# Optimization experiments

Hardware: AMD Instinct MI355X
Metric: run time of the kernel (lower is better)

Reference implementation:

```python
import jax, jax.numpy as jnp
import numpy as np

GROUP_SIZE = 128
# AWQ nibble unpack order: reverse_awq_order = [0,4,1,5,2,6,3,7]; shifts = order*4
AWQ_SHIFTS = jnp.array([0, 16, 4, 20, 8, 24, 12, 28], dtype=jnp.int32)


def awq_dequantize(qweight, scales, qzeros, group_size=GROUP_SIZE):
    # qweight: [K, N//8] int32, scales: [K//g, N] f32, qzeros: [K//g, N//8] int32
    K = qweight.shape[0]
    N = scales.shape[1]
    # unpack 8 4-bit values per int32 in AWQ order -> [K, N]
    w = ((qweight[:, :, None] >> AWQ_SHIFTS) & 15).reshape(K, N).astype(scales.dtype)
    z = ((qzeros[:, :, None] >> AWQ_SHIFTS) & 15).reshape(-1, N).astype(scales.dtype)
    # broadcast per-group scales/zeros along the K (row) axis
    z_full = jnp.repeat(z, group_size, axis=0)       # [K, N]
    s_full = jnp.repeat(scales, group_size, axis=0)  # [K, N]
    return (w - z_full) * s_full                      # [K, N]


def setup_inputs() -> dict:
    key = jax.random.key(0)
    k1, k2, k3, k4 = jax.random.split(key, 4)
    K, N, g = 4096, 11008, GROUP_SIZE
    x = jax.random.normal(k1, (4096, K), dtype=jnp.float32)
    qweight = jax.random.randint(k2, (K, N // 8), 0, 2147483647, dtype=jnp.int32)
    scales = jax.random.uniform(k3, (K // g, N), dtype=jnp.float32) * 0.01
    qzeros = jax.random.randint(k4, (K // g, N // 8), 0, 2147483647, dtype=jnp.int32)
    return {"x": x, "qweight": qweight, "scales": scales, "qzeros": qzeros}


def reference(x, qweight, scales, qzeros):
    # F.linear(x, W_deq.T) == x @ W_deq, W_deq: [K, N]
    w_deq = awq_dequantize(qweight, scales, qzeros)
    return x @ w_deq  # [tokens, N]
```

## Files before the change

kernel.cpp:

```cpp
#include <hip/hip_runtime.h>
#include <hip/hip_fp16.h>
#include <stdint.h>
#include <stddef.h>

#define MM 4096
#define NN 11008
#define KK 4096
#define NQ (NN / 8)

#define BM 256
#define BN 256
#define BK 32
#define NKT (KK / BK)
#define GRID_N (NN / BN)
#define GRID_M (MM / BM)
#define NWG (GRID_N * GRID_M)

typedef _Float16 half8 __attribute__((ext_vector_type(8)));
typedef _Float16 half2v __attribute__((ext_vector_type(2)));
typedef float f32x4 __attribute__((ext_vector_type(4)));
typedef uint32_t uint4v __attribute__((ext_vector_type(4)));

union U1H2 { uint32_t u; half2v h; };
union U4H8 { uint4v u; half8 h; };

__device__ __forceinline__ void gload_lds16(const void* g, void* l) {
  __builtin_amdgcn_global_load_lds(
      (const __attribute__((address_space(1))) uint32_t*)g,
      (__attribute__((address_space(3))) uint32_t*)l, 16, 0, 0);
}

__global__ __launch_bounds__(256) void convert_x_kernel(const float* __restrict__ x,
                                                        _Float16* __restrict__ xh) {
  const int idx = (blockIdx.x * 256 + threadIdx.x) * 8;
  const float4* p = reinterpret_cast<const float4*>(x + idx);
  float4 a = p[0], b = p[1];
  U4H8 r;
  r.h[0] = (_Float16)a.x; r.h[1] = (_Float16)a.y;
  r.h[2] = (_Float16)a.z; r.h[3] = (_Float16)a.w;
  r.h[4] = (_Float16)b.x; r.h[5] = (_Float16)b.y;
  r.h[6] = (_Float16)b.z; r.h[7] = (_Float16)b.w;
  *reinterpret_cast<uint4v*>(xh + idx) = r.u;
}

__global__ __launch_bounds__(256) void dequant_w_kernel(const uint32_t* __restrict__ qw,
                                                        const float* __restrict__ sc,
                                                        const uint32_t* __restrict__ qz,
                                                        _Float16* __restrict__ w1) {
  const int T = blockIdx.x * 256 + threadIdx.x;
  const int qc = T % NQ;
  const int kb8 = T / NQ;
  const int g = kb8 >> 4;

  const uint32_t* qp = qw + (size_t)(kb8 * 8) * NQ + qc;
  uint32_t q[8];
#pragma unroll
  for (int j = 0; j < 8; ++j) q[j] = qp[(size_t)j * NQ];

  const uint32_t zq = qz[(size_t)g * NQ + qc];
  const float* sp = sc + (size_t)g * NN + qc * 8;
  float4 s0 = *reinterpret_cast<const float4*>(sp);
  float4 s1 = *reinterpret_cast<const float4*>(sp + 4);
  const float sv[8] = {s0.x, s0.y, s0.z, s0.w, s1.x, s1.y, s1.z, s1.w};

  _Float16* op = w1 + ((size_t)kb8 * NN + (size_t)qc * 8) * 8;
#pragma unroll
  for (int c = 0; c < 8; ++c) {
    const int sh = ((c >> 1) << 2) + ((c & 1) << 4);
    uint32_t zc = ((zq >> sh) & 15u) | 0x6400u;
    zc |= zc << 16;
    U1H2 uz; uz.u = zc;
    const _Float16 hs = (_Float16)sv[c];
    half2v s2 = {hs, hs};
    uint4v outp;
#pragma unroll
    for (int i = 0; i < 4; ++i) {
      const uint32_t lo = (q[2 * i] >> sh) & 15u;
      const uint32_t hi = (q[2 * i + 1] >> sh) & 15u;
      U1H2 uw; uw.u = lo | (hi << 16) | 0x64006400u;
      U1H2 ur; ur.h = (uw.h - uz.h) * s2;
      outp[i] = ur.u;
    }
    *reinterpret_cast<uint4v*>(op + c * 8) = outp;
  }
}

__global__ __launch_bounds__(512, 2)
void gemm_pipe(const _Float16* __restrict__ xh, const _Float16* __restrict__ w1,
               float* __restrict__ out) {
  __shared__ __align__(16) _Float16 As[4][BM][BK];
  __shared__ __align__(16) _Float16 Bs[4][4][BN][8];

  const int tid = threadIdx.x;
  const int lane = tid & 63;
  const int wid = tid >> 6;
  const int wm = wid >> 2;
  const int wn = wid & 3;
  const int lr = lane & 15;
  const int lq = lane >> 4;

  const int wg = blockIdx.x;
  const int xcd = wg & 7;
  const int j = wg >> 3;
  const int m0 = (xcd * 2 + (j & 1)) * BM;
  const int n0 = (j >> 1) * BN;

  const int ca0 = tid, ca1 = 512 + tid;
  const _Float16* aSrc0 = xh + (size_t)(m0 + (ca0 >> 2)) * KK + (ca0 & 3) * 8;
  const _Float16* aSrc1 = xh + (size_t)(m0 + (ca1 >> 2)) * KK + (ca1 & 3) * 8;
  const _Float16* bSrc0 = w1 + ((size_t)(ca0 >> 8) * NN + n0 + (ca0 & 255)) * 8;
  const _Float16* bSrc1 = w1 + ((size_t)(ca1 >> 8) * NN + n0 + (ca1 & 255)) * 8;
  const int ldsOffA0 = (wid * 64) * 8;
  const int ldsOffA1 = (512 + wid * 64) * 8;

  f32x4 acc[8][4];
  const f32x4 fz = {0.f, 0.f, 0.f, 0.f};
#pragma unroll
  for (int i = 0; i < 8; ++i)
#pragma unroll
    for (int jn = 0; jn < 4; ++jn) acc[i][jn] = fz;

#pragma unroll
  for (int t = 0; t < 3; ++t) {
    gload_lds16(aSrc0 + t * BK, (char*)&As[t][0][0] + ldsOffA0 * 2);
    gload_lds16(aSrc1 + t * BK, (char*)&As[t][0][0] + ldsOffA1 * 2);
    gload_lds16(bSrc0 + (size_t)t * NN * 32, (char*)&Bs[t][0][0][0] + ldsOffA0 * 2);
    gload_lds16(bSrc1 + (size_t)t * NN * 32, (char*)&Bs[t][0][0][0] + ldsOffA1 * 2);
  }
  asm volatile("s_waitcnt vmcnt(8)" ::: "memory");
  __builtin_amdgcn_s_barrier();
  __builtin_amdgcn_sched_barrier(0);

  for (int t = 0; t < NKT; ++t) {
    const int b = t & 3;
    const int s = (t + 3) & (NKT - 1);
    const int sb = s & 3;

    half8 af[4], bf[4];
#pragma unroll
    for (int mi = 0; mi < 4; ++mi)
      af[mi] = *reinterpret_cast<const half8*>(&As[b][wm * 128 + mi * 16 + lr][lq * 8]);
#pragma unroll
    for (int ni = 0; ni < 4; ++ni)
      bf[ni] = *reinterpret_cast<const half8*>(&Bs[b][lq][wn * 64 + ni * 16 + lr][0]);
    gload_lds16(aSrc0 + s * BK, (char*)&As[sb][0][0] + ldsOffA0 * 2);
    gload_lds16(aSrc1 + s * BK, (char*)&As[sb][0][0] + ldsOffA1 * 2);
    __builtin_amdgcn_s_barrier();
    asm volatile("s_waitcnt lgkmcnt(0)" ::: "memory");
    __builtin_amdgcn_sched_barrier(0);
    __builtin_amdgcn_s_setprio(1);
#pragma unroll
    for (int mi = 0; mi < 4; ++mi)
#pragma unroll
      for (int ni = 0; ni < 4; ++ni)
        acc[mi][ni] = __builtin_amdgcn_mfma_f32_16x16x32_f16(af[mi], bf[ni], acc[mi][ni], 0, 0, 0);
    __builtin_amdgcn_s_setprio(0);
    __builtin_amdgcn_s_barrier();
    __builtin_amdgcn_sched_barrier(0);

    half8 ag[4];
#pragma unroll
    for (int mi = 0; mi < 4; ++mi)
      ag[mi] = *reinterpret_cast<const half8*>(&As[b][wm * 128 + 64 + mi * 16 + lr][lq * 8]);
    gload_lds16(bSrc0 + (size_t)s * NN * 32, (char*)&Bs[sb][0][0][0] + ldsOffA0 * 2);
    gload_lds16(bSrc1 + (size_t)s * NN * 32, (char*)&Bs[sb][0][0][0] + ldsOffA1 * 2);
    __builtin_amdgcn_s_barrier();
    asm volatile("s_waitcnt lgkmcnt(0)" ::: "memory");
    __builtin_amdgcn_sched_barrier(0);
    __builtin_amdgcn_s_setprio(1);
#pragma unroll
    for (int mi = 0; mi < 4; ++mi)
#pragma unroll
      for (int ni = 0; ni < 4; ++ni)
        acc[4 + mi][ni] = __builtin_amdgcn_mfma_f32_16x16x32_f16(ag[mi], bf[ni], acc[4 + mi][ni], 0, 0, 0);
    __builtin_amdgcn_s_setprio(0);
    asm volatile("s_waitcnt vmcnt(8)" ::: "memory");
    __builtin_amdgcn_s_barrier();
    __builtin_amdgcn_sched_barrier(0);
  }

  float* op = out + (size_t)(m0 + wm * 128) * NN + (n0 + wn * 64);
#pragma unroll
  for (int mi = 0; mi < 8; ++mi)
#pragma unroll
    for (int ni = 0; ni < 4; ++ni)
#pragma unroll
      for (int i = 0; i < 4; ++i) {
        const int row = mi * 16 + lq * 4 + i;
        const int col = ni * 16 + lr;
        op[(size_t)row * NN + col] = acc[mi][ni][i];
      }
}

template <bool APRE>
__global__ __launch_bounds__(256)
void awq_gemm(const float* __restrict__ x, const _Float16* __restrict__ xh,
              const uint32_t* __restrict__ qw, const float* __restrict__ sc,
              const uint32_t* __restrict__ qz, float* __restrict__ out) {
  __shared__ __align__(16) _Float16 Asf[128 * 64];
  __shared__ __align__(16) _Float16 Bsf[128 * 64];

  const int tid = threadIdx.x;
  const int lane = tid & 63;
  const int wid = tid >> 6;
  const int wr = wid >> 1;
  const int wc = wid & 1;
  const int n0 = blockIdx.x * 128;
  const int m0 = blockIdx.y * 128;
  const int lr = lane & 15;
  const int lq = lane >> 4;

  const int bn = tid & 127;
  const int bh = tid >> 7;
  const int gn = n0 + bn;
  const int qc = gn >> 3;
  const int jj = gn & 7;
  const int shift = ((jj >> 1) << 2) + ((jj & 1) << 4);

  const int ar = tid >> 1;
  const int ah = tid & 1;

  f32x4 acc[4][4];
  const f32x4 fz = {0.f, 0.f, 0.f, 0.f};
#pragma unroll
  for (int i = 0; i < 4; ++i)
#pragma unroll
    for (int jn = 0; jn < 4; ++jn) acc[i][jn] = fz;

  half2v zsp = {(_Float16)0.f, (_Float16)0.f};
  half2v ssp = {(_Float16)0.f, (_Float16)0.f};

  for (int kt = 0; kt < KK / 64; ++kt) {
    const int k0 = kt * 64;
    if ((kt & 1) == 0) {
      const int g = k0 >> 7;
      const uint32_t zq = qz[(size_t)g * NQ + qc];
      uint32_t zm = ((zq >> shift) & 15u) | 0x6400u;
      zm |= zm << 16;
      U1H2 uz; uz.u = zm; zsp = uz.h;
      const float s = sc[(size_t)g * NN + gn];
      const _Float16 hs = (_Float16)s;
      ssp[0] = hs; ssp[1] = hs;
    }
    __syncthreads();
    if (APRE) {
#pragma unroll
      for (int i = 0; i < 4; ++i) {
        const int cbase = (i * 4 + wid) * 64;
        const int chunk = cbase + lane;
        const int mrow = chunk >> 3;
        const int slot = (chunk & 7) ^ (mrow & 7);
        const _Float16* gp = xh + (size_t)(m0 + mrow) * KK + k0 + slot * 8;
        gload_lds16(gp, (void*)&Asf[cbase * 8]);
      }
    } else {
      const float* xp = x + (size_t)(m0 + ar) * KK + k0 + ah * 32;
#pragma unroll
      for (int j2 = 0; j2 < 4; ++j2) {
        float4 a4 = *reinterpret_cast<const float4*>(xp + j2 * 8);
        float4 b4 = *reinterpret_cast<const float4*>(xp + j2 * 8 + 4);
        U4H8 r;
        r.h[0] = (_Float16)a4.x; r.h[1] = (_Float16)a4.y;
        r.h[2] = (_Float16)a4.z; r.h[3] = (_Float16)a4.w;
        r.h[4] = (_Float16)b4.x; r.h[5] = (_Float16)b4.y;
        r.h[6] = (_Float16)b4.z; r.h[7] = (_Float16)b4.w;
        const int slot = (ah * 4 + j2) ^ (ar & 7);
        *reinterpret_cast<uint4v*>(&Asf[ar * 64 + slot * 8]) = r.u;
      }
    }
    {
      const uint32_t* qp = qw + (size_t)(k0 + bh * 32) * NQ + qc;
#pragma unroll
      for (int f = 0; f < 4; ++f) {
        uint32_t qv[8];
#pragma unroll
        for (int jv = 0; jv < 8; ++jv) qv[jv] = qp[(size_t)(f * 8 + jv) * NQ];
        uint4v wp;
#pragma unroll
        for (int p = 0; p < 4; ++p) {
          const uint32_t lo = (qv[2 * p] >> shift) & 15u;
          const uint32_t hi = (qv[2 * p + 1] >> shift);
          const uint32_t w01 = (((hi << 16) | lo) & 0x000F000Fu) | 0x64006400u;
          U1H2 uw; uw.u = w01;
          U1H2 ur; ur.h = (uw.h - zsp) * ssp;
          wp[p] = ur.u;
        }
        const int slot = (bh * 4 + f) ^ (bn & 7);
        *reinterpret_cast<uint4v*>(&Bsf[bn * 64 + slot * 8]) = wp;
      }
    }
    __syncthreads();
#pragma unroll
    for (int kq = 0; kq < 2; ++kq) {
      half8 af[4], bf[4];
#pragma unroll
      for (int mi = 0; mi < 4; ++mi) {
        const int am = wr * 64 + mi * 16 + lr;
        const int aslot = (kq * 4 + lq) ^ (am & 7);
        af[mi] = *reinterpret_cast<const half8*>(&Asf[am * 64 + aslot * 8]);
      }
#pragma unroll
      for (int ni = 0; ni < 4; ++ni) {
        const int bn2 = wc * 64 + ni * 16 + lr;
        const int bslot = (kq * 4 + lq) ^ (bn2 & 7);
        bf[ni] = *reinterpret_cast<const half8*>(&Bsf[bn2 * 64 + bslot * 8]);
      }
#pragma unroll
      for (int mi = 0; mi < 4; ++mi)
#pragma unroll
        for (int ni = 0; ni < 4; ++ni)
          acc[mi][ni] = __builtin_amdgcn_mfma_f32_16x16x32_f16(af[mi], bf[ni], acc[mi][ni], 0, 0, 0);
    }
  }

  float* op = out + (size_t)(m0 + wr * 64) * NN + (n0 + wc * 64);
#pragma unroll
  for (int mi = 0; mi < 4; ++mi)
#pragma unroll
    for (int ni = 0; ni < 4; ++ni)
#pragma unroll
      for (int i = 0; i < 4; ++i) {
        const int row = mi * 16 + lq * 4 + i;
        const int col = ni * 16 + lr;
        op[(size_t)row * NN + col] = acc[mi][ni][i];
      }
}

extern "C" void kernel_launch(void* const* d_in, const int* in_sizes, int n_in,
                              void* d_out, int out_size, void* d_ws, size_t ws_size,
                              hipStream_t stream) {
  const float* x = (const float*)d_in[0];
  const uint32_t* qw = (const uint32_t*)d_in[1];
  const float* sc = (const float*)d_in[2];
  const uint32_t* qz = (const uint32_t*)d_in[3];
  float* out = (float*)d_out;

  const size_t xh_bytes = (size_t)MM * KK * sizeof(_Float16);
  const size_t w1_bytes = (size_t)KK * NN * sizeof(_Float16);

  if (ws_size >= xh_bytes + w1_bytes) {
    _Float16* xh = (_Float16*)d_ws;
    _Float16* w1 = (_Float16*)((char*)d_ws + xh_bytes);
    convert_x_kernel<<<(MM * KK) / (256 * 8), 256, 0, stream>>>(x, xh);
    dequant_w_kernel<<<(KK / 8) * NQ / 256, 256, 0, stream>>>(qw, sc, qz, w1);
    gemm_pipe<<<NWG, 512, 0, stream>>>(xh, w1, out);
  } else if (ws_size >= xh_bytes) {
    _Float16* xh = (_Float16*)d_ws;
    convert_x_kernel<<<(MM * KK) / (256 * 8), 256, 0, stream>>>(x, xh);
    awq_gemm<true><<<dim3(NN / 128, MM / 128), 256, 0, stream>>>(x, xh, qw, sc, qz, out);
  } else {
    awq_gemm<false><<<dim3(NN / 128, MM / 128), 256, 0, stream>>>(x, nullptr, qw, sc, qz, out);
  }
}
```

Baseline: 428.4 us.

## Pre-tile and swizzle X and dequantized W into contiguous per-tile blocks for GEMM

The conversion and dequant kernels now write fp16 X and W into a tiled, XOR-swizzled layout where each 256x32 k-tile is one contiguous 16 KB block. The pipelined GEMM then streams each tile with fully contiguous global-to-LDS loads and reads fragments from a swizzled [128][64] LDS layout to avoid bank conflicts. This targets strided global access and LDS bank conflicts in the main GEMM, at the cost of scattered writes in the prep kernels and more complex index math.

```diff
diff --git a/kernel.cpp b/kernel.cpp
--- a/kernel.cpp
+++ b/kernel.cpp
@@ -16,6 +16,8 @@
 #define GRID_M (MM / BM)
 #define NWG (GRID_N * GRID_M)
 
+#define TILE_HALFS 8192
+
 typedef _Float16 half8 __attribute__((ext_vector_type(8)));
 typedef _Float16 half2v __attribute__((ext_vector_type(2)));
 typedef float f32x4 __attribute__((ext_vector_type(4)));
@@ -28,6 +30,323 @@
   __builtin_amdgcn_global_load_lds(
       (const __attribute__((address_space(1))) uint32_t*)g,
       (__attribute__((address_space(3))) uint32_t*)l, 16, 0, 0);
+}
+
+__global__ __launch_bounds__(256) void convert_x2(const float* __restrict__ x,
+                                                  _Float16* __restrict__ xh2) {
+  const int g = blockIdx.x * 256 + threadIdx.x;
+  const int c = g & 1023;
+  const int t = (g >> 10) & 127;
+  const int pan = g >> 17;
+  const int r = c >> 3;
+  const int ps = c & 7;
+  const int u = ps ^ (r & 7);
+  const int m = pan * 256 + (u >> 2) * 128 + r;
+  const int k = t * 32 + (u & 3) * 8;
+  const float4* s = reinterpret_cast<const float4*>(x + (size_t)m * KK + k);
+  float4 a = s[0], b = s[1];
+  U4H8 o;
+  o.h[0] = (_Float16)a.x; o.h[1] = (_Float16)a.y;
+  o.h[2] = (_Float16)a.z; o.h[3] = (_Float16)a.w;
+  o.h[4] = (_Float16)b.x; o.h[5] = (_Float16)b.y;
+  o.h[6] = (_Float16)b.z; o.h[7] = (_Float16)b.w;
+  *reinterpret_cast<uint4v*>(xh2 + (size_t)g * 8) = o.u;
+}
+
+__global__ __launch_bounds__(256) void dequant_w2(const uint32_t* __restrict__ qw,
+                                                  const float* __restrict__ sc,
+                                                  const uint32_t* __restrict__ qz,
+                                                  _Float16* __restrict__ w2) {
+  const int T = blockIdx.x * 256 + threadIdx.x;
+  const int qc = T % NQ;
+  const int kb8 = T / NQ;
+  const int grp = kb8 >> 4;
+  const int t = kb8 >> 2;
+  const int kbl = kb8 & 3;
+
+  const uint32_t* qp = qw + (size_t)(kb8 * 8) * NQ + qc;
+  uint32_t q[8];
+#pragma unroll
+  for (int j = 0; j < 8; ++j) q[j] = qp[(size_t)j * NQ];
+
+  const uint32_t zq = qz[(size_t)grp * NQ + qc];
+  const float* sp = sc + (size_t)grp * NN + qc * 8;
+  float4 s0 = *reinterpret_cast<const float4*>(sp);
+  float4 s1 = *reinterpret_cast<const float4*>(sp + 4);
+  const float sv[8] = {s0.x, s0.y, s0.z, s0.w, s1.x, s1.y, s1.z, s1.w};
+
+#pragma unroll
+  for (int cc = 0; cc < 8; ++cc) {
+    const int sh = ((cc >> 1) << 2) + ((cc & 1) << 4);
+    uint32_t zc = ((zq >> sh) & 15u) | 0x6400u;
+    zc |= zc << 16;
+    U1H2 uz; uz.u = zc;
+    const _Float16 hs = (_Float16)sv[cc];
+    half2v s2 = {hs, hs};
+    uint4v outp;
+#pragma unroll
+    for (int i = 0; i < 4; ++i) {
+      const uint32_t lo = (q[2 * i] >> sh) & 15u;
+      const uint32_t hi = (q[2 * i + 1] >> sh) & 15u;
+      U1H2 uw; uw.u = lo | (hi << 16) | 0x64006400u;
+      U1H2 ur; ur.h = (uw.h - uz.h) * s2;
+      outp[i] = ur.u;
+    }
+    const int n = qc * 8 + cc;
+    const int np = n >> 8;
+    const int nn = n & 255;
+    const int r = nn & 127;
+    const int h = nn >> 7;
+    const int p = (h * 4 + kbl) ^ (r & 7);
+    const size_t chunk = (((size_t)np * 128 + t) << 10) + (r << 3) + p;
+    *reinterpret_cast<uint4v*>(w2 + chunk * 8) = outp;
+  }
+}
+
+__global__ __launch_bounds__(512, 2)
+void gemm_pipe(const _Float16* __restrict__ xh2, const _Float16* __restrict__ w2,
+               float* __restrict__ out) {
+  __shared__ __align__(16) _Float16 As[4][128][64];
+  __shared__ __align__(16) _Float16 Bs[4][128][64];
+
+  const int tid = threadIdx.x;
+  const int lane = tid & 63;
+  const int wid = tid >> 6;
+  const int wm = wid >> 2;
+  const int wn = wid & 3;
+  const int lr = lane & 15;
+  const int lq = lane >> 4;
+
+  const int wg = blockIdx.x;
+  const int xcd = wg & 7;
+  const int j = wg >> 3;
+  const int mp = xcd * 2 + (j & 1);
+  const int np = j >> 1;
+  const int m0 = mp * BM;
+  const int n0 = np * BN;
+
+  const _Float16* aT = xh2 + (size_t)mp * NKT * TILE_HALFS;
+  const _Float16* bT = w2 + (size_t)np * NKT * TILE_HALFS;
+  const size_t sOff0 = (size_t)tid * 8;
+  const size_t sOff1 = (size_t)(512 + tid) * 8;
+  const int dOff0 = wid * 1024;
+  const int dOff1 = 8192 + wid * 1024;
+
+  const int pa = (wm * 4 + lq) ^ (lr & 7);
+  const int pb = ((wn >> 1) * 4 + lq) ^ (lr & 7);
+  const int rb = (wn & 1) * 64;
+
+  f32x4 acc[8][4];
+  const f32x4 fz = {0.f, 0.f, 0.f, 0.f};
+#pragma unroll
+  for (int i = 0; i < 8; ++i)
+#pragma unroll
+    for (int jn = 0; jn < 4; ++jn) acc[i][jn] = fz;
+
+#pragma unroll
+  for (int t = 0; t < 3; ++t) {
+    gload_lds16(aT + (size_t)t * TILE_HALFS + sOff0, (char*)&As[t][0][0] + dOff0);
+    gload_lds16(aT + (size_t)t * TILE_HALFS + sOff1, (char*)&As[t][0][0] + dOff1);
+    gload_lds16(bT + (size_t)t * TILE_HALFS + sOff0, (char*)&Bs[t][0][0] + dOff0);
+    gload_lds16(bT + (size_t)t * TILE_HALFS + sOff1, (char*)&Bs[t][0][0] + dOff1);
+  }
+  asm volatile("s_waitcnt vmcnt(8)" ::: "memory");
+  __builtin_amdgcn_s_barrier();
+  __builtin_amdgcn_sched_barrier(0);
+
+  for (int t = 0; t < NKT; ++t) {
+    const int b = t & 3;
+    const int s = (t + 3) & (NKT - 1);
+    const int sb = s & 3;
+
+    half8 af[4], bf[4];
+#pragma unroll
+    for (int mi = 0; mi < 4; ++mi)
+      af[mi] = *reinterpret_cast<const half8*>(&As[b][mi * 16 + lr][pa * 8]);
+#pragma unroll
+    for (int ni = 0; ni < 4; ++ni)
+      bf[ni] = *reinterpret_cast<const half8*>(&Bs[b][rb + ni * 16 + lr][pb * 8]);
+    gload_lds16(aT + (size_t)s * TILE_HALFS + sOff0, (char*)&As[sb][0][0] + dOff0);
+    gload_lds16(aT + (size_t)s * TILE_HALFS + sOff1, (char*)&As[sb][0][0] + dOff1);
+    __builtin_amdgcn_s_barrier();
+    asm volatile("s_waitcnt lgkmcnt(0)" ::: "memory");
+    __builtin_amdgcn_sched_barrier(0);
+    __builtin_amdgcn_s_setprio(1);
+#pragma unroll
+    for (int mi = 0; mi < 4; ++mi)
+#pragma unroll
+      for (int ni = 0; ni < 4; ++ni)
+        acc[mi][ni] = __builtin_amdgcn_mfma_f32_16x16x32_f16(af[mi], bf[ni], acc[mi][ni], 0, 0, 0);
+    __builtin_amdgcn_s_setprio(0);
+    __builtin_amdgcn_s_barrier();
+    __builtin_amdgcn_sched_barrier(0);
+
+    half8 ag[4];
+#pragma unroll
+    for (int mi = 0; mi < 4; ++mi)
+      ag[mi] = *reinterpret_cast<const half8*>(&As[b][64 + mi * 16 + lr][pa * 8]);
+    gload_lds16(bT + (size_t)s * TILE_HALFS + sOff0, (char*)&Bs[sb][0][0] + dOff0);
+    gload_lds16(bT + (size_t)s * TILE_HALFS + sOff1, (char*)&Bs[sb][0][0] + dOff1);
+    __builtin_amdgcn_s_barrier();
+    asm volatile("s_waitcnt lgkmcnt(0)" ::: "memory");
+    __builtin_amdgcn_sched_barrier(0);
+    __builtin_amdgcn_s_setprio(1);
+#pragma unroll
+    for (int mi = 0; mi < 4; ++mi)
+#pragma unroll
+      for (int ni = 0; ni < 4; ++ni)
+        acc[4 + mi][ni] = __builtin_amdgcn_mfma_f32_16x16x32_f16(ag[mi], bf[ni], acc[4 + mi][ni], 0, 0, 0);
+    __builtin_amdgcn_s_setprio(0);
+    asm volatile("s_waitcnt vmcnt(8)" ::: "memory");
+    __builtin_amdgcn_s_barrier();
+    __builtin_amdgcn_sched_barrier(0);
+  }
+
+  float* op = out + (size_t)(m0 + wm * 128) * NN + (n0 + wn * 64);
+#pragma unroll
+  for (int mi = 0; mi < 8; ++mi)
+#pragma unroll
+    for (int ni = 0; ni < 4; ++ni)
+#pragma unroll
+      for (int i = 0; i < 4; ++i) {
+        const int row = mi * 16 + lq * 4 + i;
+        const int col = ni * 16 + lr;
+        op[(size_t)row * NN + col] = acc[mi][ni][i];
+      }
+}
+
+template <bool APRE>
+__global__ __launch_bounds__(256)
+void awq_gemm(const float* __restrict__ x, const _Float16* __restrict__ xh,
+              const uint32_t* __restrict__ qw, const float* __restrict__ sc,
+              const uint32_t* __restrict__ qz, float* __restrict__ out) {
+  __shared__ __align__(16) _Float16 Asf[128 * 64];
+  __shared__ __align__(16) _Float16 Bsf[128 * 64];
+
+  const int tid = threadIdx.x;
+  const int lane = tid & 63;
+  const int wid = tid >> 6;
+  const int wr = wid >> 1;
+  const int wc = wid & 1;
+  const int n0 = blockIdx.x * 128;
+  const int m0 = blockIdx.y * 128;
+  const int lr = lane & 15;
+  const int lq = lane >> 4;
+
+  const int bn = tid & 127;
+  const int bh = tid >> 7;
+  const int gn = n0 + bn;
+  const int qc = gn >> 3;
+  const int jj = gn & 7;
+  const int shift = ((jj >> 1) << 2) + ((jj & 1) << 4);
+
+  const int ar = tid >> 1;
+  const int ah = tid & 1;
+
+  f32x4 acc[4][4];
+  const f32x4 fz = {0.f, 0.f, 0.f, 0.f};
+#pragma unroll
+  for (int i = 0; i < 4; ++i)
+#pragma unroll
+    for (int jn = 0; jn < 4; ++jn) acc[i][jn] = fz;
+
+  half2v zsp = {(_Float16)0.f, (_Float16)0.f};
+  half2v ssp = {(_Float16)0.f, (_Float16)0.f};
+
+  for (int kt = 0; kt < KK / 64; ++kt) {
+    const int k0 = kt * 64;
+    if ((kt & 1) == 0) {
+      const int g = k0 >> 7;
+      const uint32_t zq = qz[(size_t)g * NQ + qc];
+      uint32_t zm = ((zq >> shift) & 15u) | 0x6400u;
+      zm |= zm << 16;
+      U1H2 uz; uz.u = zm; zsp = uz.h;
+      const float s = sc[(size_t)g * NN + gn];
+      const _Float16 hs = (_Float16)s;
+      ssp[0] = hs; ssp[1] = hs;
+    }
+    __syncthreads();
+    if (APRE) {
+#pragma unroll
+      for (int i = 0; i < 4; ++i) {
+        const int cbase = (i * 4 + wid) * 64;
+        const int chunk = cbase + lane;
+        const int mrow = chunk >> 3;
+        const int slot = (chunk & 7) ^ (mrow & 7);
+        const _Float16* gp = xh + (size_t)(m0 + mrow) * KK + k0 + slot * 8;
+        gload_lds16(gp, (void*)&Asf[cbase * 8]);
+      }
+    } else {
+      const float* xp = x + (size_t)(m0 + ar) * KK + k0 + ah * 32;
+#pragma unroll
+      for (int j2 = 0; j2 < 4; ++j2) {
+        float4 a4 = *reinterpret_cast<const float4*>(xp + j2 * 8);
+        float4 b4 = *reinterpret_cast<const float4*>(xp + j2 * 8 + 4);
+        U4H8 r;
+        r.h[0] = (_Float16)a4.x; r.h[1] = (_Float16)a4.y;
+        r.h[2] = (_Float16)a4.z; r.h[3] = (_Float16)a4.w;
+        r.h[4] = (_Float16)b4.x; r.h[5] = (_Float16)b4.y;
+        r.h[6] = (_Float16)b4.z; r.h[7] = (_Float16)b4.w;
+        const int slot = (ah * 4 + j2) ^ (ar & 7);
+        *reinterpret_cast<uint4v*>(&Asf[ar * 64 + slot * 8]) = r.u;
+      }
+    }
+    {
+      const uint32_t* qp = qw + (size_t)(k0 + bh * 32) * NQ + qc;
+#pragma unroll
+      for (int f = 0; f < 4; ++f) {
+        uint32_t qv[8];
+#pragma unroll
+        for (int jv = 0; jv < 8; ++jv) qv[jv] = qp[(size_t)(f * 8 + jv) * NQ];
+        uint4v wp;
+#pragma unroll
+        for (int p = 0; p < 4; ++p) {
+          const uint32_t lo = (qv[2 * p] >> shift) & 15u;
+          const uint32_t hi = (qv[2 * p + 1] >> shift);
+          const uint32_t w01 = (((hi << 16) | lo) & 0x000F000Fu) | 0x64006400u;
+          U1H2 uw; uw.u = w01;
+          U1H2 ur; ur.h = (uw.h - zsp) * ssp;
+          wp[p] = ur.u;
+        }
+        const int slot = (bh * 4 + f) ^ (bn & 7);
+        *reinterpret_cast<uint4v*>(&Bsf[bn * 64 + slot * 8]) = wp;
+      }
+    }
+    __syncthreads();
+#pragma unroll
+    for (int kq = 0; kq < 2; ++kq) {
+      half8 af[4], bf[4];
+#pragma unroll
+      for (int mi = 0; mi < 4; ++mi) {
+        const int am = wr * 64 + mi * 16 + lr;
+        const int aslot = (kq * 4 + lq) ^ (am & 7);
+        af[mi] = *reinterpret_cast<const half8*>(&Asf[am * 64 + aslot * 8]);
+      }
+#pragma unroll
+      for (int ni = 0; ni < 4; ++ni) {
+        const int bn2 = wc * 64 + ni * 16 + lr;
+        const int bslot = (kq * 4 + lq) ^ (bn2 & 7);
+        bf[ni] = *reinterpret_cast<const half8*>(&Bsf[bn2 * 64 + bslot * 8]);
+      }
+#pragma unroll
+      for (int mi = 0; mi < 4; ++mi)
+#pragma unroll
+        for (int ni = 0; ni < 4; ++ni)
+          acc[mi][ni] = __builtin_amdgcn_mfma_f32_16x16x32_f16(af[mi], bf[ni], acc[mi][ni], 0, 0, 0);
+    }
+  }
+
+  float* op = out + (size_t)(m0 + wr * 64) * NN + (n0 + wc * 64);
+#pragma unroll
+  for (int mi = 0; mi < 4; ++mi)
+#pragma unroll
+    for (int ni = 0; ni < 4; ++ni)
+#pragma unroll
+      for (int i = 0; i < 4; ++i) {
+        const int row = mi * 16 + lq * 4 + i;
+        const int col = ni * 16 + lr;
+        op[(size_t)row * NN + col] = acc[mi][ni][i];
+      }
 }
 
 __global__ __launch_bounds__(256) void convert_x_kernel(const float* __restrict__ x,
@@ -43,289 +362,6 @@
   *reinterpret_cast<uint4v*>(xh + idx) = r.u;
 }
 
-__global__ __launch_bounds__(256) void dequant_w_kernel(const uint32_t* __restrict__ qw,
-                                                        const float* __restrict__ sc,
-                                                        const uint32_t* __restrict__ qz,
-                                                        _Float16* __restrict__ w1) {
-  const int T = blockIdx.x * 256 + threadIdx.x;
-  const int qc = T % NQ;
-  const int kb8 = T / NQ;
-  const int g = kb8 >> 4;
-
-  const uint32_t* qp = qw + (size_t)(kb8 * 8) * NQ + qc;
-  uint32_t q[8];
-#pragma unroll
-  for (int j = 0; j < 8; ++j) q[j] = qp[(size_t)j * NQ];
-
-  const uint32_t zq = qz[(size_t)g * NQ + qc];
-  const float* sp = sc + (size_t)g * NN + qc * 8;
-  float4 s0 = *reinterpret_cast<const float4*>(sp);
-  float4 s1 = *reinterpret_cast<const float4*>(sp + 4);
-  const float sv[8] = {s0.x, s0.y, s0.z, s0.w, s1.x, s1.y, s1.z, s1.w};
-
-  _Float16* op = w1 + ((size_t)kb8 * NN + (size_t)qc * 8) * 8;
-#pragma unroll
-  for (int c = 0; c < 8; ++c) {
-    const int sh = ((c >> 1) << 2) + ((c & 1) << 4);
-    uint32_t zc = ((zq >> sh) & 15u) | 0x6400u;
-    zc |= zc << 16;
-    U1H2 uz; uz.u = zc;
-    const _Float16 hs = (_Float16)sv[c];
-    half2v s2 = {hs, hs};
-    uint4v outp;
-#pragma unroll
-    for (int i = 0; i < 4; ++i) {
-      const uint32_t lo = (q[2 * i] >> sh) & 15u;
-      const uint32_t hi = (q[2 * i + 1] >> sh) & 15u;
-      U1H2 uw; uw.u = lo | (hi << 16) | 0x64006400u;
-      U1H2 ur; ur.h = (uw.h - uz.h) * s2;
-      outp[i] = ur.u;
-    }
-    *reinterpret_cast<uint4v*>(op + c * 8) = outp;
-  }
-}
-
-__global__ __launch_bounds__(512, 2)
-void gemm_pipe(const _Float16* __restrict__ xh, const _Float16* __restrict__ w1,
-               float* __restrict__ out) {
-  __shared__ __align__(16) _Float16 As[4][BM][BK];
-  __shared__ __align__(16) _Float16 Bs[4][4][BN][8];
-
-  const int tid = threadIdx.x;
-  const int lane = tid & 63;
-  const int wid = tid >> 6;
-  const int wm = wid >> 2;
-  const int wn = wid & 3;
-  const int lr = lane & 15;
-  const int lq = lane >> 4;
-
-  const int wg = blockIdx.x;
-  const int xcd = wg & 7;
-  const int j = wg >> 3;
-  const int m0 = (xcd * 2 + (j & 1)) * BM;
-  const int n0 = (j >> 1) * BN;
-
-  const int ca0 = tid, ca1 = 512 + tid;
-  const _Float16* aSrc0 = xh + (size_t)(m0 + (ca0 >> 2)) * KK + (ca0 & 3) * 8;
-  const _Float16* aSrc1 = xh + (size_t)(m0 + (ca1 >> 2)) * KK + (ca1 & 3) * 8;
-  const _Float16* bSrc0 = w1 + ((size_t)(ca0 >> 8) * NN + n0 + (ca0 & 255)) * 8;
-  const _Float16* bSrc1 = w1 + ((size_t)(ca1 >> 8) * NN + n0 + (ca1 & 255)) * 8;
-  const int ldsOffA0 = (wid * 64) * 8;
-  const int ldsOffA1 = (512 + wid * 64) * 8;
-
-  f32x4 acc[8][4];
-  const f32x4 fz = {0.f, 0.f, 0.f, 0.f};
-#pragma unroll
-  for (int i = 0; i < 8; ++i)
-#pragma unroll
-    for (int jn = 0; jn < 4; ++jn) acc[i][jn] = fz;
-
-#pragma unroll
-  for (int t = 0; t < 3; ++t) {
-    gload_lds16(aSrc0 + t * BK, (char*)&As[t][0][0] + ldsOffA0 * 2);
-    gload_lds16(aSrc1 + t * BK, (char*)&As[t][0][0] + ldsOffA1 * 2);
-    gload_lds16(bSrc0 + (size_t)t * NN * 32, (char*)&Bs[t][0][0][0] + ldsOffA0 * 2);
-    gload_lds16(bSrc1 + (size_t)t * NN * 32, (char*)&Bs[t][0][0][0] + ldsOffA1 * 2);
-  }
-  asm volatile("s_waitcnt vmcnt(8)" ::: "memory");
-  __builtin_amdgcn_s_barrier();
-  __builtin_amdgcn_sched_barrier(0);
-
-  for (int t = 0; t < NKT; ++t) {
-    const int b = t & 3;
-    const int s = (t + 3) & (NKT - 1);
-    const int sb = s & 3;
-
-    half8 af[4], bf[4];
-#pragma unroll
-    for (int mi = 0; mi < 4; ++mi)
-      af[mi] = *reinterpret_cast<const half8*>(&As[b][wm * 128 + mi * 16 + lr][lq * 8]);
-#pragma unroll
-    for (int ni = 0; ni < 4; ++ni)
-      bf[ni] = *reinterpret_cast<const half8*>(&Bs[b][lq][wn * 64 + ni * 16 + lr][0]);
-    gload_lds16(aSrc0 + s * BK, (char*)&As[sb][0][0] + ldsOffA0 * 2);
-    gload_lds16(aSrc1 + s * BK, (char*)&As[sb][0][0] + ldsOffA1 * 2);
-    __builtin_amdgcn_s_barrier();
-    asm volatile("s_waitcnt lgkmcnt(0)" ::: "memory");
-    __builtin_amdgcn_sched_barrier(0);
-    __builtin_amdgcn_s_setprio(1);
-#pragma unroll
-    for (int mi = 0; mi < 4; ++mi)
-#pragma unroll
-      for (int ni = 0; ni < 4; ++ni)
-        acc[mi][ni] = __builtin_amdgcn_mfma_f32_16x16x32_f16(af[mi], bf[ni], acc[mi][ni], 0, 0, 0);
-    __builtin_amdgcn_s_setprio(0);
-    __builtin_amdgcn_s_barrier();
-    __builtin_amdgcn_sched_barrier(0);
-
-    half8 ag[4];
-#pragma unroll
-    for (int mi = 0; mi < 4; ++mi)
-      ag[mi] = *reinterpret_cast<const half8*>(&As[b][wm * 128 + 64 + mi * 16 + lr][lq * 8]);
-    gload_lds16(bSrc0 + (size_t)s * NN * 32, (char*)&Bs[sb][0][0][0] + ldsOffA0 * 2);
-    gload_lds16(bSrc1 + (size_t)s * NN * 32, (char*)&Bs[sb][0][0][0] + ldsOffA1 * 2);
-    __builtin_amdgcn_s_barrier();
-    asm volatile("s_waitcnt lgkmcnt(0)" ::: "memory");
-    __builtin_amdgcn_sched_barrier(0);
-    __builtin_amdgcn_s_setprio(1);
-#pragma unroll
-    for (int mi = 0; mi < 4; ++mi)
-#pragma unroll
-      for (int ni = 0; ni < 4; ++ni)
-        acc[4 + mi][ni] = __builtin_amdgcn_mfma_f32_16x16x32_f16(ag[mi], bf[ni], acc[4 + mi][ni], 0, 0, 0);
-    __builtin_amdgcn_s_setprio(0);
-    asm volatile("s_waitcnt vmcnt(8)" ::: "memory");
-    __builtin_amdgcn_s_barrier();
-    __builtin_amdgcn_sched_barrier(0);
-  }
-
-  float* op = out + (size_t)(m0 + wm * 128) * NN + (n0 + wn * 64);
-#pragma unroll
-  for (int mi = 0; mi < 8; ++mi)
-#pragma unroll
-    for (int ni = 0; ni < 4; ++ni)
-#pragma unroll
-      for (int i = 0; i < 4; ++i) {
-        const int row = mi * 16 + lq * 4 + i;
-        const int col = ni * 16 + lr;
-        op[(size_t)row * NN + col] = acc[mi][ni][i];
-      }
-}
-
-template <bool APRE>
-__global__ __launch_bounds__(256)
-void awq_gemm(const float* __restrict__ x, const _Float16* __restrict__ xh,
-              const uint32_t* __restrict__ qw, const float* __restrict__ sc,
-              const uint32_t* __restrict__ qz, float* __restrict__ out) {
-  __shared__ __align__(16) _Float16 Asf[128 * 64];
-  __shared__ __align__(16) _Float16 Bsf[128 * 64];
-
-  const int tid = threadIdx.x;
-  const int lane = tid & 63;
-  const int wid = tid >> 6;
-  const int wr = wid >> 1;
-  const int wc = wid & 1;
-  const int n0 = blockIdx.x * 128;
-  const int m0 = blockIdx.y * 128;
-  const int lr = lane & 15;
-  const int lq = lane >> 4;
-
-  const int bn = tid & 127;
-  const int bh = tid >> 7;
-  const int gn = n0 + bn;
-  const int qc = gn >> 3;
-  const int jj = gn & 7;
-  const int shift = ((jj >> 1) << 2) + ((jj & 1) << 4);
-
-  const int ar = tid >> 1;
-  const int ah = tid & 1;
-
-  f32x4 acc[4][4];
-  const f32x4 fz = {0.f, 0.f, 0.f, 0.f};
-#pragma unroll
-  for (int i = 0; i < 4; ++i)
-#pragma unroll
-    for (int jn = 0; jn < 4; ++jn) acc[i][jn] = fz;
-
-  half2v zsp = {(_Float16)0.f, (_Float16)0.f};
-  half2v ssp = {(_Float16)0.f, (_Float16)0.f};
-
-  for (int kt = 0; kt < KK / 64; ++kt) {
-    const int k0 = kt * 64;
-    if ((kt & 1) == 0) {
-      const int g = k0 >> 7;
-      const uint32_t zq = qz[(size_t)g * NQ + qc];
-      uint32_t zm = ((zq >> shift) & 15u) | 0x6400u;
-      zm |= zm << 16;
-      U1H2 uz; uz.u = zm; zsp = uz.h;
-      const float s = sc[(size_t)g * NN + gn];
-      const _Float16 hs = (_Float16)s;
-      ssp[0] = hs; ssp[1] = hs;
-    }
-    __syncthreads();
-    if (APRE) {
-#pragma unroll
-      for (int i = 0; i < 4; ++i) {
-        const int cbase = (i * 4 + wid) * 64;
-        const int chunk = cbase + lane;
-        const int mrow = chunk >> 3;
-        const int slot = (chunk & 7) ^ (mrow & 7);
-        const _Float16* gp = xh + (size_t)(m0 + mrow) * KK + k0 + slot * 8;
-        gload_lds16(gp, (void*)&Asf[cbase * 8]);
-      }
-    } else {
-      const float* xp = x + (size_t)(m0 + ar) * KK + k0 + ah * 32;
-#pragma unroll
-      for (int j2 = 0; j2 < 4; ++j2) {
-        float4 a4 = *reinterpret_cast<const float4*>(xp + j2 * 8);
-        float4 b4 = *reinterpret_cast<const float4*>(xp + j2 * 8 + 4);
-        U4H8 r;
-        r.h[0] = (_Float16)a4.x; r.h[1] = (_Float16)a4.y;
-        r.h[2] = (_Float16)a4.z; r.h[3] = (_Float16)a4.w;
-        r.h[4] = (_Float16)b4.x; r.h[5] = (_Float16)b4.y;
-        r.h[6] = (_Float16)b4.z; r.h[7] = (_Float16)b4.w;
-        const int slot = (ah * 4 + j2) ^ (ar & 7);
-        *reinterpret_cast<uint4v*>(&Asf[ar * 64 + slot * 8]) = r.u;
-      }
-    }
-    {
-      const uint32_t* qp = qw + (size_t)(k0 + bh * 32) * NQ + qc;
-#pragma unroll
-      for (int f = 0; f < 4; ++f) {
-        uint32_t qv[8];
-#pragma unroll
-        for (int jv = 0; jv < 8; ++jv) qv[jv] = qp[(size_t)(f * 8 + jv) * NQ];
-        uint4v wp;
-#pragma unroll
-        for (int p = 0; p < 4; ++p) {
-          const uint32_t lo = (qv[2 * p] >> shift) & 15u;
-          const uint32_t hi = (qv[2 * p + 1] >> shift);
-          const uint32_t w01 = (((hi << 16) | lo) & 0x000F000Fu) | 0x64006400u;
-          U1H2 uw; uw.u = w01;
-          U1H2 ur; ur.h = (uw.h - zsp) * ssp;
-          wp[p] = ur.u;
-        }
-        const int slot = (bh * 4 + f) ^ (bn & 7);
-        *reinterpret_cast<uint4v*>(&Bsf[bn * 64 + slot * 8]) = wp;
-      }
-    }
-    __syncthreads();
-#pragma unroll
-    for (int kq = 0; kq < 2; ++kq) {
-      half8 af[4], bf[4];
-#pragma unroll
-      for (int mi = 0; mi < 4; ++mi) {
-        const int am = wr * 64 + mi * 16 + lr;
-        const int aslot = (kq * 4 + lq) ^ (am & 7);
-        af[mi] = *reinterpret_cast<const half8*>(&Asf[am * 64 + aslot * 8]);
-      }
-#pragma unroll
-      for (int ni = 0; ni < 4; ++ni) {
-        const int bn2 = wc * 64 + ni * 16 + lr;
-        const int bslot = (kq * 4 + lq) ^ (bn2 & 7);
-        bf[ni] = *reinterpret_cast<const half8*>(&Bsf[bn2 * 64 + bslot * 8]);
-      }
-#pragma unroll
-      for (int mi = 0; mi < 4; ++mi)
-#pragma unroll
-        for (int ni = 0; ni < 4; ++ni)
-          acc[mi][ni] = __builtin_amdgcn_mfma_f32_16x16x32_f16(af[mi], bf[ni], acc[mi][ni], 0, 0, 0);
-    }
-  }
-
-  float* op = out + (size_t)(m0 + wr * 64) * NN + (n0 + wc * 64);
-#pragma unroll
-  for (int mi = 0; mi < 4; ++mi)
-#pragma unroll
-    for (int ni = 0; ni < 4; ++ni)
-#pragma unroll
-      for (int i = 0; i < 4; ++i) {
-        const int row = mi * 16 + lq * 4 + i;
-        const int col = ni * 16 + lr;
-        op[(size_t)row * NN + col] = acc[mi][ni][i];
-      }
-}
-
 extern "C" void kernel_launch(void* const* d_in, const int* in_sizes, int n_in,
                               void* d_out, int out_size, void* d_ws, size_t ws_size,
                               hipStream_t stream) {
@@ -339,11 +375,11 @@
   const size_t w1_bytes = (size_t)KK * NN * sizeof(_Float16);
 
   if (ws_size >= xh_bytes + w1_bytes) {
-    _Float16* xh = (_Float16*)d_ws;
-    _Float16* w1 = (_Float16*)((char*)d_ws + xh_bytes);
-    convert_x_kernel<<<(MM * KK) / (256 * 8), 256, 0, stream>>>(x, xh);
-    dequant_w_kernel<<<(KK / 8) * NQ / 256, 256, 0, stream>>>(qw, sc, qz, w1);
-    gemm_pipe<<<NWG, 512, 0, stream>>>(xh, w1, out);
+    _Float16* xh2 = (_Float16*)d_ws;
+    _Float16* w2 = (_Float16*)((char*)d_ws + xh_bytes);
+    convert_x2<<<(GRID_M * NKT * 1024) / 256, 256, 0, stream>>>(x, xh2);
+    dequant_w2<<<(KK / 8) * NQ / 256, 256, 0, stream>>>(qw, sc, qz, w2);
+    gemm_pipe<<<NWG, 512, 0, stream>>>(xh2, w2, out);
   } else if (ws_size >= xh_bytes) {
     _Float16* xh = (_Float16*)d_ws;
     convert_x_kernel<<<(MM * KK) / (256 * 8), 256, 0, stream>>>(x, xh);
```

New measurement: 523.5 us. 22.2% more time.

## Double-buffer 64-wide K tiles with XOR-swizzled A layout in GEMM pipeline

Applied to the files above, without the earlier changes.

Changes the fp16 GEMM main loop from a 4-deep ring of BK=32 tiles to a double-buffered BK=64 scheme, using a single flat LDS array. The A tile is stored with an XOR swizzle on the 8-element chunk index to reduce LDS bank conflicts on fragment reads. Each 64-wide tile runs as four compute phases that interleave global-to-LDS staging of the next tile, with finer vmcnt waits. This halves the loop trip count and the barriers per K element, at the cost of a shallower prefetch depth (two buffers instead of four).

```diff
diff --git a/kernel.cpp b/kernel.cpp
--- a/kernel.cpp
+++ b/kernel.cpp
@@ -10,11 +10,13 @@
 
 #define BM 256
 #define BN 256
-#define BK 32
+#define BK 64
 #define NKT (KK / BK)
 #define GRID_N (NN / BN)
 #define GRID_M (MM / BM)
 #define NWG (GRID_N * GRID_M)
+
+#define HT 8192
 
 typedef _Float16 half8 __attribute__((ext_vector_type(8)));
 typedef _Float16 half2v __attribute__((ext_vector_type(2)));
@@ -88,8 +90,7 @@
 __global__ __launch_bounds__(512, 2)
 void gemm_pipe(const _Float16* __restrict__ xh, const _Float16* __restrict__ w1,
                float* __restrict__ out) {
-  __shared__ __align__(16) _Float16 As[4][BM][BK];
-  __shared__ __align__(16) _Float16 Bs[4][4][BN][8];
+  __shared__ __align__(16) _Float16 S[65536];
 
   const int tid = threadIdx.x;
   const int lane = tid & 63;
@@ -105,13 +106,17 @@
   const int m0 = (xcd * 2 + (j & 1)) * BM;
   const int n0 = (j >> 1) * BN;
 
-  const int ca0 = tid, ca1 = 512 + tid;
-  const _Float16* aSrc0 = xh + (size_t)(m0 + (ca0 >> 2)) * KK + (ca0 & 3) * 8;
-  const _Float16* aSrc1 = xh + (size_t)(m0 + (ca1 >> 2)) * KK + (ca1 & 3) * 8;
-  const _Float16* bSrc0 = w1 + ((size_t)(ca0 >> 8) * NN + n0 + (ca0 & 255)) * 8;
-  const _Float16* bSrc1 = w1 + ((size_t)(ca1 >> 8) * NN + n0 + (ca1 & 255)) * 8;
-  const int ldsOffA0 = (wid * 64) * 8;
-  const int ldsOffA1 = (512 + wid * 64) * 8;
+  const int c0 = tid, c1 = 512 + tid;
+  const _Float16* aS0 = xh + (size_t)(m0 + (c0 >> 2)) * KK
+                           + ((c0 & 3) ^ ((c0 >> 3) & 3)) * 8;
+  const _Float16* aS1 = xh + (size_t)(m0 + (c1 >> 2)) * KK
+                           + ((c1 & 3) ^ ((c1 >> 3) & 3)) * 8;
+  const _Float16* bS0 = w1 + ((size_t)(c0 >> 8) * NN + n0 + (c0 & 255)) * 8;
+  const _Float16* bS1 = w1 + ((size_t)(c1 >> 8) * NN + n0 + (c1 & 255)) * 8;
+
+  const int sa8 = (lq ^ ((lr >> 1) & 3)) * 8;
+  const int vA = (wm * 128 + lr) * 32 + sa8;
+  const int vB = lq * 2048 + (wn * 64 + lr) * 8;
 
   f32x4 acc[8][4];
   const f32x4 fz = {0.f, 0.f, 0.f, 0.f};
@@ -120,64 +125,94 @@
 #pragma unroll
     for (int jn = 0; jn < 4; ++jn) acc[i][jn] = fz;
 
-#pragma unroll
-  for (int t = 0; t < 3; ++t) {
-    gload_lds16(aSrc0 + t * BK, (char*)&As[t][0][0] + ldsOffA0 * 2);
-    gload_lds16(aSrc1 + t * BK, (char*)&As[t][0][0] + ldsOffA1 * 2);
-    gload_lds16(bSrc0 + (size_t)t * NN * 32, (char*)&Bs[t][0][0][0] + ldsOffA0 * 2);
-    gload_lds16(bSrc1 + (size_t)t * NN * 32, (char*)&Bs[t][0][0][0] + ldsOffA1 * 2);
-  }
-  asm volatile("s_waitcnt vmcnt(8)" ::: "memory");
-  __builtin_amdgcn_s_barrier();
-  __builtin_amdgcn_sched_barrier(0);
-
-  for (int t = 0; t < NKT; ++t) {
-    const int b = t & 3;
-    const int s = (t + 3) & (NKT - 1);
-    const int sb = s & 3;
-
-    half8 af[4], bf[4];
-#pragma unroll
-    for (int mi = 0; mi < 4; ++mi)
-      af[mi] = *reinterpret_cast<const half8*>(&As[b][wm * 128 + mi * 16 + lr][lq * 8]);
-#pragma unroll
-    for (int ni = 0; ni < 4; ++ni)
-      bf[ni] = *reinterpret_cast<const half8*>(&Bs[b][lq][wn * 64 + ni * 16 + lr][0]);
-    gload_lds16(aSrc0 + s * BK, (char*)&As[sb][0][0] + ldsOffA0 * 2);
-    gload_lds16(aSrc1 + s * BK, (char*)&As[sb][0][0] + ldsOffA1 * 2);
-    __builtin_amdgcn_s_barrier();
-    asm volatile("s_waitcnt lgkmcnt(0)" ::: "memory");
-    __builtin_amdgcn_sched_barrier(0);
-    __builtin_amdgcn_s_setprio(1);
-#pragma unroll
-    for (int mi = 0; mi < 4; ++mi)
-#pragma unroll
-      for (int ni = 0; ni < 4; ++ni)
-        acc[mi][ni] = __builtin_amdgcn_mfma_f32_16x16x32_f16(af[mi], bf[ni], acc[mi][ni], 0, 0, 0);
-    __builtin_amdgcn_s_setprio(0);
-    __builtin_amdgcn_s_barrier();
-    __builtin_amdgcn_sched_barrier(0);
-
-    half8 ag[4];
-#pragma unroll
-    for (int mi = 0; mi < 4; ++mi)
-      ag[mi] = *reinterpret_cast<const half8*>(&As[b][wm * 128 + 64 + mi * 16 + lr][lq * 8]);
-    gload_lds16(bSrc0 + (size_t)s * NN * 32, (char*)&Bs[sb][0][0][0] + ldsOffA0 * 2);
-    gload_lds16(bSrc1 + (size_t)s * NN * 32, (char*)&Bs[sb][0][0][0] + ldsOffA1 * 2);
-    __builtin_amdgcn_s_barrier();
-    asm volatile("s_waitcnt lgkmcnt(0)" ::: "memory");
-    __builtin_amdgcn_sched_barrier(0);
-    __builtin_amdgcn_s_setprio(1);
-#pragma unroll
-    for (int mi = 0; mi < 4; ++mi)
-#pragma unroll
-      for (int ni = 0; ni < 4; ++ni)
-        acc[4 + mi][ni] = __builtin_amdgcn_mfma_f32_16x16x32_f16(ag[mi], bf[ni], acc[4 + mi][ni], 0, 0, 0);
-    __builtin_amdgcn_s_setprio(0);
-    asm volatile("s_waitcnt vmcnt(8)" ::: "memory");
-    __builtin_amdgcn_s_barrier();
-    __builtin_amdgcn_sched_barrier(0);
-  }
+  half8 af[4], bf[4], bf2[4];
+
+#define RD_A4(BUF, KKX, MIH)                                                   \
+  _Pragma("unroll") for (int mi = 0; mi < 4; ++mi)                             \
+      af[mi] = *reinterpret_cast<const half8*>(                                \
+          &S[((BUF) * 2 + (KKX)) * HT + ((MIH) + mi) * 512 + vA]);
+
+#define RD_B4(BUF, KKX, REG)                                                   \
+  _Pragma("unroll") for (int ni = 0; ni < 4; ++ni)                             \
+      REG[ni] = *reinterpret_cast<const half8*>(                               \
+          &S[32768 + ((BUF) * 2 + (KKX)) * HT + ni * 128 + vB]);
+
+#define MF16(ACCH, REG)                                                        \
+  _Pragma("unroll") for (int mi = 0; mi < 4; ++mi)                             \
+      _Pragma("unroll") for (int ni = 0; ni < 4; ++ni)                         \
+          acc[(ACCH) + mi][ni] = __builtin_amdgcn_mfma_f32_16x16x32_f16(       \
+              af[mi], REG[ni], acc[(ACCH) + mi][ni], 0, 0, 0);
+
+#define STG_A(KKX, BUFX, AOFF)                                                 \
+  gload_lds16(aS0 + (AOFF) + (KKX) * 32,                                       \
+              &S[((BUFX) * 2 + (KKX)) * HT + wid * 512]);                      \
+  gload_lds16(aS1 + (AOFF) + (KKX) * 32,                                       \
+              &S[((BUFX) * 2 + (KKX)) * HT + 4096 + wid * 512]);
+
+#define STG_B(KKX, BUFX, BOFF)                                                 \
+  gload_lds16(bS0 + (BOFF) + (size_t)(KKX) * NN * 32,                          \
+              &S[32768 + ((BUFX) * 2 + (KKX)) * HT + wid * 512]);              \
+  gload_lds16(bS1 + (BOFF) + (size_t)(KKX) * NN * 32,                          \
+              &S[32768 + ((BUFX) * 2 + (KKX)) * HT + 4096 + wid * 512]);
+
+#define BARRIER __builtin_amdgcn_s_barrier()
+#define LGKM0 asm volatile("s_waitcnt lgkmcnt(0)" ::: "memory")
+#define VMC(N) asm volatile("s_waitcnt vmcnt(" #N ")" ::: "memory")
+#define SB0 __builtin_amdgcn_sched_barrier(0)
+#define PRIO1 __builtin_amdgcn_s_setprio(1)
+#define PRIO0 __builtin_amdgcn_s_setprio(0)
+
+#define TILE64(T, BUF)                                                         \
+  {                                                                            \
+    const size_t aOff = (size_t)(((T) + 1) & (NKT - 1)) * BK;                  \
+    const size_t bOff = (size_t)(((T) + 1) & (NKT - 1)) * ((size_t)NN * 64);   \
+                                                                       \
+    RD_A4(BUF, 0, 0)                                                           \
+    RD_B4(BUF, 0, bf)                                                          \
+    STG_A(0, (BUF) ^ 1, aOff)                                                  \
+    BARRIER; LGKM0; SB0;                                                       \
+    PRIO1; MF16(0, bf) PRIO0;                                                  \
+    BARRIER; SB0;                                                              \
+                                                                       \
+    RD_A4(BUF, 0, 4)                                                           \
+    STG_B(0, (BUF) ^ 1, bOff)                                                  \
+    VMC(6); BARRIER; LGKM0; SB0;                                               \
+    PRIO1; MF16(4, bf) PRIO0;                                                  \
+    BARRIER; SB0;                                                              \
+                                                                       \
+    RD_A4(BUF, 1, 0)                                                           \
+    RD_B4(BUF, 1, bf2)                                                         \
+    STG_A(1, (BUF) ^ 1, aOff)                                                  \
+    VMC(6); BARRIER; LGKM0; SB0;                                               \
+    PRIO1; MF16(0, bf2) PRIO0;                                                 \
+    BARRIER; SB0;                                                              \
+                                                                       \
+    RD_A4(BUF, 1, 4)                                                           \
+    STG_B(1, (BUF) ^ 1, bOff)                                                  \
+    VMC(4); BARRIER; LGKM0; SB0;                                               \
+    PRIO1; MF16(4, bf2) PRIO0;                                                 \
+    BARRIER; SB0;                                                              \
+  }
+
+  STG_A(0, 0, 0)
+  STG_B(0, 0, 0)
+  STG_A(1, 0, 0)
+  STG_B(1, 0, 0)
+  VMC(4);
+  BARRIER; SB0;
+
+  for (int it = 0; it < NKT / 2; ++it) {
+    const int t0 = it * 2;
+    TILE64(t0, 0)
+    TILE64(t0 + 1, 1)
+  }
+
+#undef TILE64
+#undef RD_A4
+#undef RD_B4
+#undef MF16
+#undef STG_A
+#undef STG_B
 
   float* op = out + (size_t)(m0 + wm * 128) * NN + (n0 + wn * 64);
 #pragma unroll
```

After: 389.7 us. 9.0% less time.
